# Kernel tuning notes

Hardware: AMD Instinct MI355X
Metric: run time of the kernel (lower is better)

Reference implementation:

```python
import jax, jax.numpy as jnp
import numpy as np

# Static graph/model dims
G, NPG, N = 64, 200, 12800          # graphs, nodes/graph, total nodes
EPG, E = 1000, 64000                # edges/graph, total edges
D, H, C = 1024, 3, 1024             # feature_size, heads, out channels/head
K1, K2, K3 = 160, 80, 16            # topk sizes: ceil(.8*200), .5*160, .2*80
NEG = -1e9


def _gat(x, src, dst, mask, W, att_s, att_d, b):
    """PyG GATConv (concat heads, add_self_loops=True, leaky_relu 0.2)."""
    n = x.shape[0]
    xw = (x @ W).reshape(n, H, C)                 # [n,H,C]
    a_s = (xw * att_s).sum(-1)                    # [n,H]
    a_d = (xw * att_d).sum(-1)
    loop = jnp.arange(n, dtype=src.dtype)
    s = jnp.concatenate([src, loop])
    d = jnp.concatenate([dst, loop])
    m = jnp.concatenate([mask, jnp.ones((n,), bool)])
    logit = jax.nn.leaky_relu(a_s[s] + a_d[d], 0.2)   # [E+n,H]
    logit = jnp.where(m[:, None], logit, NEG)
    mx = jax.ops.segment_max(logit, d, num_segments=n)
    ex = jnp.where(m[:, None], jnp.exp(logit - mx[d]), 0.0)
    den = jax.ops.segment_sum(ex, d, num_segments=n)
    alpha = ex / (den[d] + 1e-16)                 # segment softmax over dst
    out = jax.ops.segment_sum(alpha[:, :, None] * xw[s], d, num_segments=n)
    return out.reshape(n, H * C) + b


def _topk(x, src, dst, mask, p, n_in, k):
    """PyG TopKPooling: score=tanh(x.p/||p||), keep top-k per graph,
    scale kept rows by score; edge filtering realized as a mask."""
    score = jnp.tanh((x @ p) / jnp.linalg.norm(p))
    vals, idx = jax.lax.top_k(score.reshape(G, n_in), k)     # [G,k]
    perm = (idx + jnp.arange(G)[:, None] * n_in).reshape(-1)
    new_x = x[perm] * vals.reshape(-1, 1)
    newid = jnp.full((G * n_in,), -1, jnp.int32).at[perm].set(
        jnp.arange(G * k, dtype=jnp.int32))
    ns, nd = newid[src], newid[dst]
    nm = mask & (ns >= 0) & (nd >= 0)
    return new_x, jnp.where(nm, ns, 0), jnp.where(nm, nd, 0), nm


def _readout(x, k):
    xg = x.reshape(G, k, C)                       # contiguous equal graphs
    return jnp.concatenate([xg.max(1), xg.mean(1)], axis=1)  # [G,2C]


def setup_inputs() -> dict:
    key = jax.random.key(0)
    ks = jax.random.split(key, 32)
    x = jax.random.normal(ks[0], (N, D), jnp.float32)
    gid = jnp.repeat(jnp.arange(G, dtype=jnp.int32), EPG)
    src = jax.random.randint(ks[1], (E,), 0, NPG, jnp.int32) + gid * NPG
    dst = jax.random.randint(ks[2], (E,), 0, NPG, jnp.int32) + gid * NPG
    edge_index = jnp.stack([src, dst])
    batch_index = jnp.repeat(jnp.arange(G, dtype=jnp.int32), NPG)
    edge_attr = jnp.zeros((E, 1), jnp.float32)

    def gl(k, shape, fan):
        return jax.random.normal(k, shape, jnp.float32) * (1.0 / np.sqrt(fan))

    inp = dict(x=x, edge_attr=edge_attr, edge_index=edge_index,
               batch_index=batch_index)
    i = 3
    for L, fin in ((1, D), (2, C), (3, C)):
        inp[f'W{L}'] = gl(ks[i], (fin, H * C), fin); i += 1
        inp[f'as{L}'] = gl(ks[i], (H, C), C); i += 1
        inp[f'ad{L}'] = gl(ks[i], (H, C), C); i += 1
        inp[f'b{L}'] = jnp.zeros((H * C,), jnp.float32)
        inp[f'Wt{L}'] = gl(ks[i], (H * C, C), H * C); i += 1
        inp[f'bt{L}'] = jnp.zeros((C,), jnp.float32)
        inp[f'p{L}'] = gl(ks[i], (C,), C); i += 1
    inp['Wl1'] = gl(ks[i], (2 * C, 1024), 2 * C); i += 1
    inp['bl1'] = jnp.zeros((1024,), jnp.float32)
    inp['Wl2'] = gl(ks[i], (1024, 2), 1024); i += 1
    inp['bl2'] = jnp.zeros((2,), jnp.float32)
    return inp


def reference(x, edge_attr, edge_index, batch_index,
              W1, as1, ad1, b1, Wt1, bt1, p1,
              W2, as2, ad2, b2, Wt2, bt2, p2,
              W3, as3, ad3, b3, Wt3, bt3, p3,
              Wl1, bl1, Wl2, bl2):
    src, dst = edge_index[0], edge_index[1]
    mask = jnp.ones((src.shape[0],), bool)
    h = _gat(x, src, dst, mask, W1, as1, ad1, b1) @ Wt1 + bt1
    h, src, dst, mask = _topk(h, src, dst, mask, p1, NPG, K1)
    r1 = _readout(h, K1)
    h = _gat(h, src, dst, mask, W2, as2, ad2, b2) @ Wt2 + bt2
    h, src, dst, mask = _topk(h, src, dst, mask, p2, K1, K2)
    r2 = _readout(h, K2)
    h = _gat(h, src, dst, mask, W3, as3, ad3, b3) @ Wt3 + bt3
    h, src, dst, mask = _topk(h, src, dst, mask, p3, K2, K3)
    r3 = _readout(h, K3)
    z = r1 + r2 + r3                               # [G, 2C]
    z = jax.nn.relu(z @ Wl1 + bl1)                 # dropout inactive (eval)
    return z @ Wl2 + bl2                           # [G, 2]
```

## Files before the change

### kernel.cpp

```cpp
#include <hip/hip_runtime.h>
#include <math.h>

#define NG 64
#define EE 64000
#define HC3 3072
#define CC 1024

static inline int cdiv(int a, int b) { return (a + b - 1) / b; }

typedef float f4_t __attribute__((ext_vector_type(4)));
typedef short s8_t __attribute__((ext_vector_type(8)));

__device__ __forceinline__ float lrelu(float x) { return x > 0.f ? x : 0.2f * x; }
__device__ __forceinline__ unsigned fenc(float f) {
    unsigned u = __float_as_uint(f);
    return (u & 0x80000000u) ? ~u : (u | 0x80000000u);
}
__device__ __forceinline__ float fdec(unsigned e) {
    return (e & 0x80000000u) ? __uint_as_float(e ^ 0x80000000u) : __uint_as_float(~e);
}
__device__ __forceinline__ unsigned short f2bf(float f) {
    unsigned u = __float_as_uint(f);
    u += 0x7fffu + ((u >> 16) & 1u);
    return (unsigned short)(u >> 16);
}
__device__ __forceinline__ float bf2f(unsigned short h) {
    return __uint_as_float(((unsigned)h) << 16);
}
__device__ __forceinline__ void gll16(const unsigned short* g, unsigned short* l) {
    __builtin_amdgcn_global_load_lds(
        (const __attribute__((address_space(1))) void*)g,
        (__attribute__((address_space(3))) void*)l, 16, 0, 0);
}

__global__ __launch_bounds__(256) void gemm_prep(
    const unsigned short* __restrict__ Ahi, const unsigned short* __restrict__ Alo,
    const unsigned short* __restrict__ Bhi, const unsigned short* __restrict__ Blo,
    unsigned short* __restrict__ ohi, unsigned short* __restrict__ olo, int K)
{
    __shared__ unsigned short sAH[128 * 32];
    __shared__ unsigned short sAL[128 * 32];
    __shared__ unsigned short sBH[128 * 32];
    __shared__ unsigned short sBL[128 * 32];

    const size_t MSZ = (size_t)CC * CC;
    const int slot = blockIdx.z;
    const int lrel = slot / 3, hh = slot % 3;
    Ahi += slot * MSZ; Alo += slot * MSZ;
    Bhi += slot * MSZ; Blo += slot * MSZ;

    const int t = threadIdx.x;
    const int w = t >> 6, lane = t & 63;
    const int wr = w >> 1, wc = w & 1;
    const int row0 = blockIdx.y * 128, col0 = blockIdx.x * 128;

    const int srow = w * 16 + (lane >> 2);
    const int skg = (((lane & 3) ^ ((lane >> 3) & 3)) << 3);
    const size_t aoff0 = (size_t)(row0 + srow) * CC + skg;
    const size_t aoff1 = (size_t)(row0 + 64 + srow) * CC + skg;
    const size_t boff0 = (size_t)(col0 + srow) * CC + skg;
    const size_t boff1 = (size_t)(col0 + 64 + srow) * CC + skg;
    const int l0 = (w * 16) * 32;
    const int l1 = (64 + w * 16) * 32;

    f4_t acc[4][4];
    const f4_t z4 = {0.f, 0.f, 0.f, 0.f};
#pragma unroll
    for (int i = 0; i < 4; ++i)
#pragma unroll
        for (int j = 0; j < 4; ++j) acc[i][j] = z4;

    const int mrow0 = wr * 64 + (lane & 15);
    const int nrow0 = wc * 64 + (lane & 15);
    const int kslot = (((lane >> 4) ^ ((lane >> 1) & 3)) << 3);

    for (int k0 = 0; k0 < K; k0 += 32) {
        gll16(Ahi + aoff0 + k0, &sAH[l0]);
        gll16(Ahi + aoff1 + k0, &sAH[l1]);
        gll16(Alo + aoff0 + k0, &sAL[l0]);
        gll16(Alo + aoff1 + k0, &sAL[l1]);
        gll16(Bhi + boff0 + k0, &sBH[l0]);
        gll16(Bhi + boff1 + k0, &sBH[l1]);
        gll16(Blo + boff0 + k0, &sBL[l0]);
        gll16(Blo + boff1 + k0, &sBL[l1]);
        __syncthreads();

        s8_t ah[4], al[4], bh[4], bl[4];
#pragma unroll
        for (int mt = 0; mt < 4; ++mt) {
            ah[mt] = *(const s8_t*)&sAH[(mrow0 + mt * 16) * 32 + kslot];
            al[mt] = *(const s8_t*)&sAL[(mrow0 + mt * 16) * 32 + kslot];
        }
#pragma unroll
        for (int nt = 0; nt < 4; ++nt) {
            bh[nt] = *(const s8_t*)&sBH[(nrow0 + nt * 16) * 32 + kslot];
            bl[nt] = *(const s8_t*)&sBL[(nrow0 + nt * 16) * 32 + kslot];
        }
#pragma unroll
        for (int mt = 0; mt < 4; ++mt)
#pragma unroll
            for (int nt = 0; nt < 4; ++nt) {
                acc[mt][nt] = __builtin_amdgcn_mfma_f32_16x16x32_bf16(ah[mt], bh[nt], acc[mt][nt], 0, 0, 0);
                acc[mt][nt] = __builtin_amdgcn_mfma_f32_16x16x32_bf16(ah[mt], bl[nt], acc[mt][nt], 0, 0, 0);
                acc[mt][nt] = __builtin_amdgcn_mfma_f32_16x16x32_bf16(al[mt], bh[nt], acc[mt][nt], 0, 0, 0);
            }
        __syncthreads();
    }

#pragma unroll
    for (int mt = 0; mt < 4; ++mt) {
        int row = row0 + wr * 64 + mt * 16 + (lane >> 4) * 4;
#pragma unroll
        for (int nt = 0; nt < 4; ++nt) {
            int col = col0 + wc * 64 + nt * 16 + (lane & 15);
#pragma unroll
            for (int r = 0; r < 4; ++r) {
                float v = acc[mt][nt][r];
                unsigned short hv = f2bf(v);
                size_t dst = (size_t)lrel * 3 * MSZ + (size_t)(row + r) * HC3 + hh * CC + col;
                ohi[dst] = hv;
                olo[dst] = f2bf(v - bf2f(hv));
            }
        }
    }
}

__global__ __launch_bounds__(256) void gemm_splitk(
    const unsigned short* __restrict__ Ahi, const unsigned short* __restrict__ Alo, int lda,
    const unsigned short* __restrict__ Bhi, const unsigned short* __restrict__ Blo, int ldb,
    float* __restrict__ C, int ldc, int ksub)
{
    __shared__ unsigned short sAH[128 * 32];
    __shared__ unsigned short sAL[128 * 32];
    __shared__ unsigned short sBH[128 * 32];
    __shared__ unsigned short sBL[128 * 32];

    const int t = threadIdx.x;
    const int w = t >> 6, lane = t & 63;
    const int wr = w >> 1, wc = w & 1;
    const int row0 = blockIdx.x * 128, col0 = blockIdx.y * 128;
    const int kbase = blockIdx.z * ksub;

    const int srow = w * 16 + (lane >> 2);
    const int skg = (((lane & 3) ^ ((lane >> 3) & 3)) << 3);
    const size_t aoff0 = (size_t)(row0 + srow) * lda + skg;
    const size_t aoff1 = (size_t)(row0 + 64 + srow) * lda + skg;
    const size_t boff0 = (size_t)(col0 + srow) * ldb + skg;
    const size_t boff1 = (size_t)(col0 + 64 + srow) * ldb + skg;
    const int l0 = (w * 16) * 32;
    const int l1 = (64 + w * 16) * 32;

    f4_t acc[4][4];
    const f4_t z4 = {0.f, 0.f, 0.f, 0.f};
#pragma unroll
    for (int i = 0; i < 4; ++i)
#pragma unroll
        for (int j = 0; j < 4; ++j) acc[i][j] = z4;

    const int mrow0 = wr * 64 + (lane & 15);
    const int nrow0 = wc * 64 + (lane & 15);
    const int kslot = (((lane >> 4) ^ ((lane >> 1) & 3)) << 3);

    for (int k0 = kbase; k0 < kbase + ksub; k0 += 32) {
        gll16(Ahi + aoff0 + k0, &sAH[l0]);
        gll16(Ahi + aoff1 + k0, &sAH[l1]);
        gll16(Alo + aoff0 + k0, &sAL[l0]);
        gll16(Alo + aoff1 + k0, &sAL[l1]);
        gll16(Bhi + boff0 + k0, &sBH[l0]);
        gll16(Bhi + boff1 + k0, &sBH[l1]);
        gll16(Blo + boff0 + k0, &sBL[l0]);
        gll16(Blo + boff1 + k0, &sBL[l1]);
        __syncthreads();

        s8_t ah[4], al[4], bh[4], bl[4];
#pragma unroll
        for (int mt = 0; mt < 4; ++mt) {
            ah[mt] = *(const s8_t*)&sAH[(mrow0 + mt * 16) * 32 + kslot];
            al[mt] = *(const s8_t*)&sAL[(mrow0 + mt * 16) * 32 + kslot];
        }
#pragma unroll
        for (int nt = 0; nt < 4; ++nt) {
            bh[nt] = *(const s8_t*)&sBH[(nrow0 + nt * 16) * 32 + kslot];
            bl[nt] = *(const s8_t*)&sBL[(nrow0 + nt * 16) * 32 + kslot];
        }
#pragma unroll
        for (int mt = 0; mt < 4; ++mt)
#pragma unroll
            for (int nt = 0; nt < 4; ++nt) {
                acc[mt][nt] = __builtin_amdgcn_mfma_f32_16x16x32_bf16(ah[mt], bh[nt], acc[mt][nt], 0, 0, 0);
                acc[mt][nt] = __builtin_amdgcn_mfma_f32_16x16x32_bf16(ah[mt], bl[nt], acc[mt][nt], 0, 0, 0);
                acc[mt][nt] = __builtin_amdgcn_mfma_f32_16x16x32_bf16(al[mt], bh[nt], acc[mt][nt], 0, 0, 0);
            }
        __syncthreads();
    }

#pragma unroll
    for (int mt = 0; mt < 4; ++mt) {
        int row = row0 + wr * 64 + mt * 16 + (lane >> 4) * 4;
#pragma unroll
        for (int nt = 0; nt < 4; ++nt) {
            int col = col0 + wc * 64 + nt * 16 + (lane & 15);
#pragma unroll
            for (int r = 0; r < 4; ++r)
                atomicAdd(&C[(size_t)(row + r) * ldc + col], acc[mt][nt][r]);
        }
    }
}

__global__ void split_w_all(const float* __restrict__ w0, const float* __restrict__ w1,
    const float* __restrict__ w2, int lbase,
    unsigned short* __restrict__ ohi, unsigned short* __restrict__ olo)
{
    const float* Wp[3] = {w0, w1, w2};
    int slot = blockIdx.y;
    int L = lbase + slot / 3, h = slot % 3;
    int idx = blockIdx.x * 256 + threadIdx.x;
    int r = idx >> 10, c = idx & 1023;
    float v = Wp[L][(size_t)r * HC3 + h * CC + c];
    unsigned short hh = f2bf(v);
    ohi[(size_t)slot * 1048576 + idx] = hh;
    olo[(size_t)slot * 1048576 + idx] = f2bf(v - bf2f(hh));
}

__global__ void transpose_split_wt_all(const float* __restrict__ w0,
    const float* __restrict__ w1, const float* __restrict__ w2, int lbase,
    unsigned short* __restrict__ ohi, unsigned short* __restrict__ olo)
{
    const float* Wp[3] = {w0, w1, w2};
    int slot = blockIdx.z;
    int L = lbase + slot / 3, h = slot % 3;
    __shared__ float tile[32][33];
    int t = threadIdx.x, tr = t >> 5, tc = t & 31;
    int r0 = blockIdx.y * 32, c0 = blockIdx.x * 32;
    const float* in = Wp[L] + (size_t)h * 1048576;
#pragma unroll
    for (int i = 0; i < 4; ++i)
        tile[tr + i * 8][tc] = in[(size_t)(r0 + tr + i * 8) * CC + c0 + tc];
    __syncthreads();
    unsigned short* oh = ohi + (size_t)slot * 1048576;
    unsigned short* ol = olo + (size_t)slot * 1048576;
#pragma unroll
    for (int i = 0; i < 4; ++i) {
        int oc = c0 + tr + i * 8;
        int orr = r0 + tc;
        float v = tile[tc][tr + i * 8];
        unsigned short hh = f2bf(v);
        oh[(size_t)oc * CC + orr] = hh;
        ol[(size_t)oc * CC + orr] = f2bf(v - bf2f(hh));
    }
}

__global__ __launch_bounds__(256) void wtp_all(const float* __restrict__ wt0,
    const float* __restrict__ wt1, const float* __restrict__ wt2,
    const float* __restrict__ p0, const float* __restrict__ p1, const float* __restrict__ p2,
    int lbase, float* __restrict__ U)
{
    const float* Wp[3] = {wt0, wt1, wt2};
    const float* Pp[3] = {p0, p1, p2};
    int wid = blockIdx.x * 4 + (threadIdx.x >> 6);
    int lane = threadIdx.x & 63;
    int L = lbase + wid / HC3, rr = wid % HC3;
    const float* row = Wp[L] + (size_t)rr * CC;
    const float* p = Pp[L];
    float s = 0.f;
    for (int c = lane; c < CC; c += 64) s += row[c] * p[c];
    for (int off = 32; off; off >>= 1) s += __shfl_xor(s, off, 64);
    if (lane == 0) U[(size_t)L * HC3 + rr] = s;
}

__global__ __launch_bounds__(256) void attvec_all(const float* __restrict__ w0,
    const float* __restrict__ w1, const float* __restrict__ w2,
    const float* __restrict__ as0, const float* __restrict__ as1, const float* __restrict__ as2,
    const float* __restrict__ ad0, const float* __restrict__ ad1, const float* __restrict__ ad2,
    const float* __restrict__ U, int lbase,
    float* __restrict__ asv, float* __restrict__ adv, float* __restrict__ qv)
{
    const float* Wp[3] = {w0, w1, w2};
    const float* Sp[3] = {as0, as1, as2};
    const float* Dp[3] = {ad0, ad1, ad2};
    int L = lbase + blockIdx.y;
    int wid = blockIdx.x * 4 + (threadIdx.x >> 6);
    int lane = threadIdx.x & 63;
    int h = wid >> 10, kk = wid & 1023;
    const float* wr = Wp[L] + (long long)kk * HC3 + h * CC;
    const float* sa = Sp[L] + h * CC;
    const float* da = Dp[L] + h * CC;
    const float* ua = U + (size_t)L * HC3 + h * CC;
    float ss = 0.f, dd = 0.f, qq = 0.f;
    for (int c = lane; c < CC; c += 64) {
        float w = wr[c];
        ss += w * sa[c]; dd += w * da[c]; qq += w * ua[c];
    }
    for (int off = 32; off; off >>= 1) {
        ss += __shfl_xor(ss, off, 64); dd += __shfl_xor(dd, off, 64); qq += __shfl_xor(qq, off, 64);
    }
    if (lane == 0) {
        asv[(size_t)L * HC3 + h * CC + kk] = ss;
        adv[(size_t)L * HC3 + h * CC + kk] = dd;
        qv[(size_t)L * HC3 + h * CC + kk] = qq;
    }
}

__global__ __launch_bounds__(256) void attn_node(const float* __restrict__ xin,
    const float* __restrict__ asv, const float* __restrict__ adv, const float* __restrict__ q,
    float* __restrict__ AS, float* __restrict__ AD, float* __restrict__ T3,
    float* __restrict__ sl, unsigned* __restrict__ mxe, float* __restrict__ sexp,
    int* __restrict__ cnt, int* __restrict__ cur, int n)
{
    int node = blockIdx.x * 4 + (threadIdx.x >> 6);
    int lane = threadIdx.x & 63;
    if (node >= n) return;
    const float* xr = xin + (long long)node * CC;
    float s0 = 0, s1 = 0, s2 = 0, d0 = 0, d1 = 0, d2 = 0, t0 = 0, t1 = 0, t2 = 0;
    for (int j = lane; j < CC; j += 64) {
        float v = xr[j];
        s0 += v * asv[j]; s1 += v * asv[CC + j]; s2 += v * asv[2 * CC + j];
        d0 += v * adv[j]; d1 += v * adv[CC + j]; d2 += v * adv[2 * CC + j];
        t0 += v * q[j];   t1 += v * q[CC + j];   t2 += v * q[2 * CC + j];
    }
    for (int off = 32; off; off >>= 1) {
        s0 += __shfl_xor(s0, off, 64); s1 += __shfl_xor(s1, off, 64); s2 += __shfl_xor(s2, off, 64);
        d0 += __shfl_xor(d0, off, 64); d1 += __shfl_xor(d1, off, 64); d2 += __shfl_xor(d2, off, 64);
        t0 += __shfl_xor(t0, off, 64); t1 += __shfl_xor(t1, off, 64); t2 += __shfl_xor(t2, off, 64);
    }
    if (lane == 0) {
        AS[node * 3 + 0] = s0; AS[node * 3 + 1] = s1; AS[node * 3 + 2] = s2;
        AD[node * 3 + 0] = d0; AD[node * 3 + 1] = d1; AD[node * 3 + 2] = d2;
        T3[node * 3 + 0] = t0; T3[node * 3 + 1] = t1; T3[node * 3 + 2] = t2;
        float l0v = lrelu(s0 + d0), l1v = lrelu(s1 + d1), l2v = lrelu(s2 + d2);
        sl[node * 3 + 0] = l0v; sl[node * 3 + 1] = l1v; sl[node * 3 + 2] = l2v;
        mxe[node * 3 + 0] = fenc(l0v); mxe[node * 3 + 1] = fenc(l1v); mxe[node * 3 + 2] = fenc(l2v);
        sexp[node * 3 + 0] = 0.f; sexp[node * 3 + 1] = 0.f; sexp[node * 3 + 2] = 0.f;
        cnt[node] = 0; cur[node] = 0;
    }
}

__global__ void bvinit_pnorm(const float* __restrict__ bt0, const float* __restrict__ bt1,
    const float* __restrict__ bt2, const float* __restrict__ p0, const float* __restrict__ p1,
    const float* __restrict__ p2, int lbase, float* __restrict__ BV, float* __restrict__ PN)
{
    const float* Bp[3] = {bt0, bt1, bt2};
    const float* Pp[3] = {p0, p1, p2};
    int L = lbase + blockIdx.y;
    if (blockIdx.x < 4) {
        int c = blockIdx.x * 256 + threadIdx.x;
        BV[(size_t)L * CC + c] = Bp[L][c];
    } else {
        __shared__ float red[256];
        int t = threadIdx.x;
        const float* p = Pp[L];
        float s = 0.f;
        for (int j = t; j < CC; j += 256) { float v = p[j]; s += v * v; }
        red[t] = s; __syncthreads();
        for (int off = 128; off; off >>= 1) { if (t < off) red[t] += red[t + off]; __syncthreads(); }
        if (t == 0) PN[L] = sqrtf(red[0]);
    }
}

__global__ void bvec_part(const float* __restrict__ b0, const float* __restrict__ b1,
    const float* __restrict__ b2, const float* __restrict__ wt0, const float* __restrict__ wt1,
    const float* __restrict__ wt2, int lbase, float* __restrict__ BV)
{
    const float* bp[3] = {b0, b1, b2};
    const float* wp[3] = {wt0, wt1, wt2};
    int L = lbase + blockIdx.z;
    int c = blockIdx.x * 256 + threadIdx.x;
    int k0 = blockIdx.y * 256;
    const float* b = bp[L];
    const float* Wt = wp[L];
    float acc = 0.f;
#pragma unroll 8
    for (int k = k0; k < k0 + 256; ++k) acc += b[k] * Wt[(size_t)k * CC + c];
    atomicAdd(&BV[(size_t)L * CC + c], acc);
}

__global__ void bvp_all(const float* __restrict__ BV, const float* __restrict__ p0,
    const float* __restrict__ p1, const float* __restrict__ p2, int lbase,
    float* __restrict__ BVP)
{
    const float* Pp[3] = {p0, p1, p2};
    int L = lbase + blockIdx.x;
    __shared__ float red[256];
    int t = threadIdx.x;
    const float* p = Pp[L];
    float s = 0.f;
    for (int j = t; j < CC; j += 256) s += BV[(size_t)L * CC + j] * p[j];
    red[t] = s; __syncthreads();
    for (int off = 128; off; off >>= 1) { if (t < off) red[t] += red[t + off]; __syncthreads(); }
    if (t == 0) BVP[L] = red[0];
}

__global__ void edge_pass1(const int* __restrict__ src, const int* __restrict__ dst,
    const int* __restrict__ msk, const float* __restrict__ AS, const float* __restrict__ AD,
    unsigned* __restrict__ mxe, float* __restrict__ sexp, int* __restrict__ cnt)
{
    int e = blockIdx.x * 256 + threadIdx.x;
    if (e >= EE || !msk[e]) return;
    int s = src[e], d = dst[e];
    atomicAdd(&cnt[d], 1);
#pragma unroll
    for (int h = 0; h < 3; ++h) {
        float l = lrelu(AS[s * 3 + h] + AD[d * 3 + h]);
        atomicMax(&mxe[d * 3 + h], fenc(l));
        atomicAdd(&sexp[d * 3 + h], expf(l));
    }
}

__global__ __launch_bounds__(64) void scan_graph(const int* __restrict__ cnt,
    int* __restrict__ offs, int* __restrict__ gt, int npg)
{
    int g = blockIdx.x, lane = threadIdx.x;
    int run = 0;
    for (int c0 = 0; c0 < npg; c0 += 64) {
        int i = c0 + lane;
        int v = (i < npg) ? cnt[g * npg + i] : 0;
        int s = v;
#pragma unroll
        for (int off = 1; off < 64; off <<= 1) {
            int o = __shfl_up(s, off, 64);
            if (lane >= off) s += o;
        }
        if (i < npg) offs[g * npg + i] = run + s - v;
        run += __shfl(s, 63, 64);
    }
    if (lane == 0) gt[g] = run;
}

__global__ void post_edge(int* __restrict__ offs, const int* __restrict__ gt,
    const unsigned* __restrict__ mxe, const float* __restrict__ sl,
    const float* __restrict__ sexp, float* __restrict__ mxf, float* __restrict__ den,
    int n, int npg)
{
    int i = blockIdx.x * 256 + threadIdx.x;
    if (i >= n) return;
    int g = i / npg;
    int base = 0;
    for (int gg = 0; gg < g; ++gg) base += gt[gg];
    offs[i] += base;
#pragma unroll
    for (int h = 0; h < 3; ++h) {
        float m = fdec(mxe[i * 3 + h]);
        mxf[i * 3 + h] = m;
        den[i * 3 + h] = expf(sl[i * 3 + h] - m) + expf(-m) * sexp[i * 3 + h];
    }
}

__global__ void fill_alpha(const int* __restrict__ src, const int* __restrict__ dst,
    const int* __restrict__ msk, const int* __restrict__ offs, int* __restrict__ cur,
    const float* __restrict__ AS, const float* __restrict__ AD,
    const float* __restrict__ mxf, const float* __restrict__ den,
    int* __restrict__ csrs, float* __restrict__ csra)
{
    int e = blockIdx.x * 256 + threadIdx.x;
    if (e >= EE || !msk[e]) return;
    int s = src[e], d = dst[e];
    int pos = offs[d] + atomicAdd(&cur[d], 1);
    csrs[pos] = s;
#pragma unroll
    for (int h = 0; h < 3; ++h) {
        float l = lrelu(AS[s * 3 + h] + AD[d * 3 + h]);
        float ex = expf(l - mxf[d * 3 + h]);
        csra[pos * 3 + h] = ex / (den[d * 3 + h] + 1e-16f);
    }
}

__global__ __launch_bounds__(64) void score_topk(const float* __restrict__ T3,
    const float* __restrict__ sl, const float* __restrict__ mxf, const float* __restrict__ den,
    const int* __restrict__ offs, const int* __restrict__ cnt, const int* __restrict__ csrs,
    const float* __restrict__ csra, const float* __restrict__ bvp, const float* __restrict__ pn,
    int npg, int k, int* __restrict__ perm, float* __restrict__ vals, int* __restrict__ newid)
{
    __shared__ float sc[256];
    int g = blockIdx.x, lane = threadIdx.x;
    float bv0 = bvp[0], pn0 = pn[0];
    for (int ii = lane; ii < npg; ii += 64) {
        int i = g * npg + ii;
        float s = 0.f;
#pragma unroll
        for (int h = 0; h < 3; ++h) {
            float aself = expf(sl[i * 3 + h] - mxf[i * 3 + h]) / (den[i * 3 + h] + 1e-16f);
            s += aself * T3[i * 3 + h];
        }
        int beg = offs[i], num = cnt[i];
        for (int e = 0; e < num; ++e) {
            int sn = csrs[beg + e];
#pragma unroll
            for (int h = 0; h < 3; ++h) s += csra[(beg + e) * 3 + h] * T3[sn * 3 + h];
        }
        sc[ii] = tanhf((s + bv0) / pn0);
        newid[i] = -1;
    }
    __syncthreads();
    float v[4];
    int nsl = (npg + 63) >> 6;
#pragma unroll
    for (int s2 = 0; s2 < 4; ++s2) {
        int idx = lane + (s2 << 6);
        v[s2] = (s2 < nsl && idx < npg) ? sc[idx] : -1e30f;
    }
    for (int j = 0; j < k; ++j) {
        float bv = -2e30f; int bi = 0x7fffffff;
#pragma unroll
        for (int s2 = 0; s2 < 4; ++s2) {
            int idx = lane + (s2 << 6);
            if (v[s2] > bv) { bv = v[s2]; bi = idx; }
        }
        for (int off = 32; off; off >>= 1) {
            float ov = __shfl_xor(bv, off, 64);
            int   oi = __shfl_xor(bi, off, 64);
            if (ov > bv || (ov == bv && oi < bi)) { bv = ov; bi = oi; }
        }
        if (lane == 0) {
            perm[g * k + j] = g * npg + bi;
            vals[g * k + j] = bv;
            newid[g * npg + bi] = g * k + j;
        }
        if ((bi & 63) == lane) v[bi >> 6] = -1e30f;
    }
}

__global__ __launch_bounds__(256) void aggregate_sel(const float* __restrict__ xin,
    const float* __restrict__ sl, const float* __restrict__ mxf, const float* __restrict__ den,
    const int* __restrict__ offs, const int* __restrict__ cnt,
    const int* __restrict__ csrs, const float* __restrict__ csra,
    const int* __restrict__ perm,
    unsigned short* __restrict__ ahi, unsigned short* __restrict__ alo)
{
    int r = blockIdx.x, t = threadIdx.x;
    int i = perm[r];
    float aself[3];
#pragma unroll
    for (int h = 0; h < 3; ++h)
        aself[h] = expf(sl[i * 3 + h] - mxf[i * 3 + h]) / (den[i * 3 + h] + 1e-16f);
    const float* xr = xin + (long long)i * CC;
    float acc[3][4];
#pragma unroll
    for (int j = 0; j < 4; ++j) {
        float v = xr[t + (j << 8)];
#pragma unroll
        for (int h = 0; h < 3; ++h) acc[h][j] = aself[h] * v;
    }
    int beg = offs[i], num = cnt[i];
    for (int e = 0; e < num; ++e) {
        int s = csrs[beg + e];
        float a0 = csra[(beg + e) * 3 + 0];
        float a1 = csra[(beg + e) * 3 + 1];
        float a2 = csra[(beg + e) * 3 + 2];
        const float* sr = xin + (long long)s * CC;
#pragma unroll
        for (int j = 0; j < 4; ++j) {
            float v = sr[t + (j << 8)];
            acc[0][j] += a0 * v; acc[1][j] += a1 * v; acc[2][j] += a2 * v;
        }
    }
#pragma unroll
    for (int h = 0; h < 3; ++h)
#pragma unroll
        for (int j = 0; j < 4; ++j) {
            int c = t + (j << 8);
            float v = acc[h][j];
            unsigned short hh = f2bf(v);
            size_t idx = (size_t)r * HC3 + h * CC + c;
            ahi[idx] = hh;
            alo[idx] = f2bf(v - bf2f(hh));
        }
}

__global__ void remap_edges(int* __restrict__ s, int* __restrict__ d,
    int* __restrict__ m, const int* __restrict__ newid)
{
    int e = blockIdx.x * 256 + threadIdx.x;
    if (e >= EE) return;
    if (!m[e]) { s[e] = 0; d[e] = 0; return; }
    int ns = newid[s[e]], nd = newid[d[e]];
    int nm = (ns >= 0 && nd >= 0) ? 1 : 0;
    m[e] = nm; s[e] = nm ? ns : 0; d[e] = nm ? nd : 0;
}

__global__ __launch_bounds__(256) void readout_part(float* __restrict__ xn,
    const float* __restrict__ BV, const float* __restrict__ vals,
    int k, float* __restrict__ PM, float* __restrict__ PS)
{
    int g = blockIdx.x, ch = blockIdx.y, t = threadIdx.x;
    int rpc = k >> 3, r0 = ch * rpc;
#pragma unroll
    for (int j = 0; j < 4; ++j) {
        int c = t + (j << 8);
        float bvc = BV[c];
        float mx = -1e30f, sm = 0.f;
        for (int r = r0; r < r0 + rpc; ++r) {
            size_t idx = ((size_t)(g * k + r)) * CC + c;
            float vv = (xn[idx] + bvc) * vals[g * k + r];
            xn[idx] = vv;
            mx = fmaxf(mx, vv); sm += vv;
        }
        PM[(size_t)(g * 8 + ch) * CC + c] = mx;
        PS[(size_t)(g * 8 + ch) * CC + c] = sm;
    }
}

__global__ __launch_bounds__(256) void readout_fin(const float* __restrict__ PM,
    const float* __restrict__ PS, int k, float* __restrict__ R)
{
    int g = blockIdx.x, t = threadIdx.x;
#pragma unroll
    for (int j = 0; j < 4; ++j) {
        int c = t + (j << 8);
        float mx = -1e30f, sm = 0.f;
#pragma unroll
        for (int ch = 0; ch < 8; ++ch) {
            mx = fmaxf(mx, PM[(size_t)(g * 8 + ch) * CC + c]);
            sm += PS[(size_t)(g * 8 + ch) * CC + c];
        }
        R[g * 2048 + c] = mx;
        R[g * 2048 + 1024 + c] = sm / (float)k;
    }
}

__global__ void copy_edges(const int* __restrict__ ei, int* __restrict__ s,
    int* __restrict__ d, int* __restrict__ m)
{
    int e = blockIdx.x * 256 + threadIdx.x;
    if (e >= EE) return;
    s[e] = ei[e]; d[e] = ei[EE + e]; m[e] = 1;
}

__global__ __launch_bounds__(256) void mlp1_kernel(const float* __restrict__ R0,
    const float* __restrict__ R1, const float* __restrict__ R2,
    const float* __restrict__ Wl1, const float* __restrict__ bl1, float* __restrict__ Z1)
{
    int c = blockIdx.x * 256 + threadIdx.x;
    int g = blockIdx.y;
    float acc = bl1[c];
    const float* r0 = R0 + g * 2048;
    const float* r1 = R1 + g * 2048;
    const float* r2 = R2 + g * 2048;
    for (int kk = 0; kk < 2048; ++kk)
        acc += (r0[kk] + r1[kk] + r2[kk]) * Wl1[kk * 1024 + c];
    Z1[g * 1024 + c] = acc > 0.f ? acc : 0.f;
}

__global__ __launch_bounds__(64) void mlp2_kernel(const float* __restrict__ Z1,
    const float* __restrict__ Wl2, const float* __restrict__ bl2, float* __restrict__ out)
{
    int b = blockIdx.x; int g = b >> 1, o = b & 1;
    int lane = threadIdx.x;
    const float* zr = Z1 + g * 1024;
    float s = 0.f;
    for (int j = lane; j < 1024; j += 64) s += zr[j] * Wl2[j * 2 + o];
    for (int off = 32; off; off >>= 1) s += __shfl_xor(s, off, 64);
    if (lane == 0) out[g * 2 + o] = s + bl2[o];
}

extern "C" void kernel_launch(void* const* d_in, const int* in_sizes, int n_in,
                              void* d_out, int out_size, void* d_ws, size_t ws_size,
                              hipStream_t stream)
{
    const float* x   = (const float*)d_in[0];
    const int*   ei  = (const int*)d_in[2];
    const float* W[3]    = {(const float*)d_in[4],  (const float*)d_in[11], (const float*)d_in[18]};
    const float* atts[3] = {(const float*)d_in[5],  (const float*)d_in[12], (const float*)d_in[19]};
    const float* attd[3] = {(const float*)d_in[6],  (const float*)d_in[13], (const float*)d_in[20]};
    const float* bb[3]   = {(const float*)d_in[7],  (const float*)d_in[14], (const float*)d_in[21]};
    const float* Wt[3]   = {(const float*)d_in[8],  (const float*)d_in[15], (const float*)d_in[22]};
    const float* bt[3]   = {(const float*)d_in[9],  (const float*)d_in[16], (const float*)d_in[23]};
    const float* pv[3]   = {(const float*)d_in[10], (const float*)d_in[17], (const float*)d_in[24]};
    const float* Wl1 = (const float*)d_in[25];
    const float* bl1 = (const float*)d_in[26];
    const float* Wl2 = (const float*)d_in[27];
    const float* bl2 = (const float*)d_in[28];
    float* out = (float*)d_out;

    const bool batched = ws_size >= (size_t)225 * 1024 * 1024;

    char* wp = (char*)d_ws;
    auto carve = [&](size_t bytes) -> void* {
        void* p = (void*)wp;
        wp += (bytes + 255) & ~(size_t)255;
        return p;
    };
    const int NMAX = 12800;
    const int GKMAX = 10240;
    const size_t MSZ = (size_t)CC * CC;
    const int NSLOT = batched ? 9 : 3;
    unsigned short* A2H = (unsigned short*)carve((size_t)GKMAX * HC3 * 2);
    unsigned short* A2L = (unsigned short*)carve((size_t)GKMAX * HC3 * 2);
    unsigned short* WTH = (unsigned short*)A2H;
    unsigned short* WTL = WTH + (size_t)NSLOT * MSZ;
    unsigned short* WSH = WTL + (size_t)NSLOT * MSZ;
    unsigned short* WSL = (unsigned short*)A2L;
    float* XN   = (float*)carve((size_t)GKMAX * CC * 4);
    unsigned short* B2H = (unsigned short*)carve((size_t)NSLOT * MSZ * 2);
    unsigned short* B2L = (unsigned short*)carve((size_t)NSLOT * MSZ * 2);
    float* PM   = (float*)carve((size_t)NG * 8 * CC * 4);
    float* PS   = (float*)carve((size_t)NG * 8 * CC * 4);
    float* ASV  = (float*)carve((size_t)3 * HC3 * 4);
    float* ADV  = (float*)carve((size_t)3 * HC3 * 4);
    float* QV   = (float*)carve((size_t)3 * HC3 * 4);
    float* UU   = (float*)carve((size_t)3 * HC3 * 4);
    float* BV   = (float*)carve((size_t)3 * CC * 4);
    float* AS   = (float*)carve((size_t)NMAX * 3 * 4);
    float* AD   = (float*)carve((size_t)NMAX * 3 * 4);
    float* T3   = (float*)carve((size_t)NMAX * 3 * 4);
    float* SL   = (float*)carve((size_t)NMAX * 3 * 4);
    unsigned* MXE = (unsigned*)carve((size_t)NMAX * 3 * 4);
    float* MXF  = (float*)carve((size_t)NMAX * 3 * 4);
    float* DEN  = (float*)carve((size_t)NMAX * 3 * 4);
    float* SEXP = (float*)carve((size_t)NMAX * 3 * 4);
    int* CNT    = (int*)carve((size_t)NMAX * 4);
    int* OFFS   = (int*)carve((size_t)NMAX * 4);
    int* CUR    = (int*)carve((size_t)NMAX * 4);
    int* NEWID  = (int*)carve((size_t)NMAX * 4);
    int* GT     = (int*)carve((size_t)NG * 4);
    int* CSRS   = (int*)carve((size_t)EE * 4);
    float* CSRA = (float*)carve((size_t)EE * 3 * 4);
    int* SRC = (int*)carve((size_t)EE * 4);
    int* DST = (int*)carve((size_t)EE * 4);
    int* MK  = (int*)carve((size_t)EE * 4);
    int* PERM  = (int*)carve((size_t)GKMAX * 4);
    float* VALS = (float*)carve((size_t)GKMAX * 4);
    float* PN  = (float*)carve(256);
    float* BVP = (float*)carve(256);
    float* R0 = (float*)carve((size_t)NG * 2048 * 4);
    float* R1 = (float*)carve((size_t)NG * 2048 * 4);
    float* R2 = (float*)carve((size_t)NG * 2048 * 4);
    float* Z1 = (float*)carve((size_t)NG * 1024 * 4);
    float* Rarr[3] = {R0, R1, R2};
    (void)in_sizes; (void)n_in; (void)out_size;

    copy_edges<<<cdiv(EE, 256), 256, 0, stream>>>(ei, SRC, DST, MK);

    auto prep = [&](int lbase, int nl) {
        int nslots = 3 * nl;
        split_w_all<<<dim3(4096, nslots), 256, 0, stream>>>(W[0], W[1], W[2], lbase, WSH, WSL);
        transpose_split_wt_all<<<dim3(32, 32, nslots), 256, 0, stream>>>(Wt[0], Wt[1], Wt[2],
                                                                          lbase, WTH, WTL);
        wtp_all<<<nl * 768, 256, 0, stream>>>(Wt[0], Wt[1], Wt[2], pv[0], pv[1], pv[2],
                                              lbase, UU);
        gemm_prep<<<dim3(8, 8, nslots), 256, 0, stream>>>(WTH, WTL, WSH, WSL, B2H, B2L, CC);
        attvec_all<<<dim3(768, nl), 256, 0, stream>>>(W[0], W[1], W[2],
            atts[0], atts[1], atts[2], attd[0], attd[1], attd[2], UU, lbase, ASV, ADV, QV);
        bvinit_pnorm<<<dim3(5, nl), 256, 0, stream>>>(bt[0], bt[1], bt[2],
            pv[0], pv[1], pv[2], lbase, BV, PN);
        bvec_part<<<dim3(4, 12, nl), 256, 0, stream>>>(bb[0], bb[1], bb[2],
            Wt[0], Wt[1], Wt[2], lbase, BV);
        bvp_all<<<nl, 256, 0, stream>>>(BV, pv[0], pv[1], pv[2], lbase, BVP);
    };

    if (batched) prep(0, 3);

    const int ns_[3]  = {12800, 10240, 5120};
    const int npg_[3] = {200, 160, 80};
    const int kk_[3]  = {160, 80, 16};
    const int sk_[3]  = {2, 2, 4};
    const float* xin = x;

    for (int L = 0; L < 3; ++L) {
        int n = ns_[L], npg = npg_[L], k = kk_[L];
        int gk = NG * k;
        if (!batched) prep(L, 1);
        size_t b2off = batched ? (size_t)L * 3 * MSZ : 0;
        attn_node<<<n / 4, 256, 0, stream>>>(xin, ASV + (size_t)L * HC3,
            ADV + (size_t)L * HC3, QV + (size_t)L * HC3, AS, AD, T3,
            SL, MXE, SEXP, CNT, CUR, n);
        edge_pass1<<<cdiv(EE, 256), 256, 0, stream>>>(SRC, DST, MK, AS, AD, MXE, SEXP, CNT);
        scan_graph<<<NG, 64, 0, stream>>>(CNT, OFFS, GT, npg);
        post_edge<<<cdiv(n, 256), 256, 0, stream>>>(OFFS, GT, MXE, SL, SEXP, MXF, DEN, n, npg);
        fill_alpha<<<cdiv(EE, 256), 256, 0, stream>>>(SRC, DST, MK, OFFS, CUR,
                                                      AS, AD, MXF, DEN, CSRS, CSRA);
        score_topk<<<NG, 64, 0, stream>>>(T3, SL, MXF, DEN, OFFS, CNT, CSRS, CSRA,
                                          BVP + L, PN + L, npg, k, PERM, VALS, NEWID);
        aggregate_sel<<<gk, 256, 0, stream>>>(xin, SL, MXF, DEN, OFFS, CNT, CSRS, CSRA,
                                              PERM, A2H, A2L);
        hipMemsetAsync(XN, 0, (size_t)gk * CC * 4, stream);
        gemm_splitk<<<dim3(gk / 128, 8, sk_[L]), 256, 0, stream>>>(A2H, A2L, HC3,
            B2H + b2off, B2L + b2off, HC3, XN, CC, HC3 / sk_[L]);
        readout_part<<<dim3(NG, 8), 256, 0, stream>>>(XN, BV + (size_t)L * CC, VALS,
                                                      k, PM, PS);
        readout_fin<<<NG, 256, 0, stream>>>(PM, PS, k, Rarr[L]);
        if (L < 2) remap_edges<<<cdiv(EE, 256), 256, 0, stream>>>(SRC, DST, MK, NEWID);
        xin = XN;
    }

    mlp1_kernel<<<dim3(4, NG), 256, 0, stream>>>(R0, R1, R2, Wl1, bl1, Z1);
    mlp2_kernel<<<NG * 2, 64, 0, stream>>>(Z1, Wl2, bl2, out);
}
```

Measured before the change: 1.335 ms.

## Replace CSR build with fixed-degree adjacency slots and recompute attention on the fly

Drops the scan/post-edge/fill-alpha kernels: edges are written directly into per-node fixed MAXDEG slots during the first edge pass, and attention coefficients are recomputed from AS/AD/max/sum in score_topk and aggregate_sel. Edge remapping for the next layer is folded into edge_pass1. This removes several small kernel launches and the CSR alpha buffer. It risks silently dropping edges if any node's in-degree exceeds 64, though the running sums still count every edge.

```diff
diff --git a/kernel.cpp b/kernel.cpp
--- a/kernel.cpp
+++ b/kernel.cpp
@@ -5,6 +5,7 @@
 #define EE 64000
 #define HC3 3072
 #define CC 1024
+#define MAXDEG 64
 
 static inline int cdiv(int a, int b) { return (a + b - 1) / b; }
 
@@ -305,7 +306,7 @@
     const float* __restrict__ asv, const float* __restrict__ adv, const float* __restrict__ q,
     float* __restrict__ AS, float* __restrict__ AD, float* __restrict__ T3,
     float* __restrict__ sl, unsigned* __restrict__ mxe, float* __restrict__ sexp,
-    int* __restrict__ cnt, int* __restrict__ cur, int n)
+    int* __restrict__ cnt, int n)
 {
     int node = blockIdx.x * 4 + (threadIdx.x >> 6);
     int lane = threadIdx.x & 63;
@@ -331,7 +332,7 @@
         sl[node * 3 + 0] = l0v; sl[node * 3 + 1] = l1v; sl[node * 3 + 2] = l2v;
         mxe[node * 3 + 0] = fenc(l0v); mxe[node * 3 + 1] = fenc(l1v); mxe[node * 3 + 2] = fenc(l2v);
         sexp[node * 3 + 0] = 0.f; sexp[node * 3 + 1] = 0.f; sexp[node * 3 + 2] = 0.f;
-        cnt[node] = 0; cur[node] = 0;
+        cnt[node] = 0;
     }
 }
 
@@ -390,14 +391,29 @@
     if (t == 0) BVP[L] = red[0];
 }
 
-__global__ void edge_pass1(const int* __restrict__ src, const int* __restrict__ dst,
-    const int* __restrict__ msk, const float* __restrict__ AS, const float* __restrict__ AD,
-    unsigned* __restrict__ mxe, float* __restrict__ sexp, int* __restrict__ cnt)
+__global__ void edge_pass1(int* __restrict__ src, int* __restrict__ dst,
+    int* __restrict__ msk, const int* __restrict__ newid,
+    const float* __restrict__ AS, const float* __restrict__ AD,
+    unsigned* __restrict__ mxe, float* __restrict__ sexp, int* __restrict__ cnt,
+    int* __restrict__ csrs)
 {
     int e = blockIdx.x * 256 + threadIdx.x;
-    if (e >= EE || !msk[e]) return;
-    int s = src[e], d = dst[e];
-    atomicAdd(&cnt[d], 1);
+    if (e >= EE) return;
+    int m = msk[e];
+    int s, d;
+    if (newid) {
+        if (!m) { src[e] = 0; dst[e] = 0; return; }
+        int ns = newid[src[e]], nd = newid[dst[e]];
+        int nm = (ns >= 0 && nd >= 0) ? 1 : 0;
+        msk[e] = nm; src[e] = nm ? ns : 0; dst[e] = nm ? nd : 0;
+        if (!nm) return;
+        s = ns; d = nd;
+    } else {
+        if (!m) return;
+        s = src[e]; d = dst[e];
+    }
+    int slot = atomicAdd(&cnt[d], 1);
+    if (slot < MAXDEG) csrs[d * MAXDEG + slot] = s;
 #pragma unroll
     for (int h = 0; h < 3; ++h) {
         float l = lrelu(AS[s * 3 + h] + AD[d * 3 + h]);
@@ -406,68 +422,11 @@
     }
 }
 
-__global__ __launch_bounds__(64) void scan_graph(const int* __restrict__ cnt,
-    int* __restrict__ offs, int* __restrict__ gt, int npg)
-{
-    int g = blockIdx.x, lane = threadIdx.x;
-    int run = 0;
-    for (int c0 = 0; c0 < npg; c0 += 64) {
-        int i = c0 + lane;
-        int v = (i < npg) ? cnt[g * npg + i] : 0;
-        int s = v;
-#pragma unroll
-        for (int off = 1; off < 64; off <<= 1) {
-            int o = __shfl_up(s, off, 64);
-            if (lane >= off) s += o;
-        }
-        if (i < npg) offs[g * npg + i] = run + s - v;
-        run += __shfl(s, 63, 64);
-    }
-    if (lane == 0) gt[g] = run;
-}
-
-__global__ void post_edge(int* __restrict__ offs, const int* __restrict__ gt,
-    const unsigned* __restrict__ mxe, const float* __restrict__ sl,
-    const float* __restrict__ sexp, float* __restrict__ mxf, float* __restrict__ den,
-    int n, int npg)
-{
-    int i = blockIdx.x * 256 + threadIdx.x;
-    if (i >= n) return;
-    int g = i / npg;
-    int base = 0;
-    for (int gg = 0; gg < g; ++gg) base += gt[gg];
-    offs[i] += base;
-#pragma unroll
-    for (int h = 0; h < 3; ++h) {
-        float m = fdec(mxe[i * 3 + h]);
-        mxf[i * 3 + h] = m;
-        den[i * 3 + h] = expf(sl[i * 3 + h] - m) + expf(-m) * sexp[i * 3 + h];
-    }
-}
-
-__global__ void fill_alpha(const int* __restrict__ src, const int* __restrict__ dst,
-    const int* __restrict__ msk, const int* __restrict__ offs, int* __restrict__ cur,
-    const float* __restrict__ AS, const float* __restrict__ AD,
-    const float* __restrict__ mxf, const float* __restrict__ den,
-    int* __restrict__ csrs, float* __restrict__ csra)
-{
-    int e = blockIdx.x * 256 + threadIdx.x;
-    if (e >= EE || !msk[e]) return;
-    int s = src[e], d = dst[e];
-    int pos = offs[d] + atomicAdd(&cur[d], 1);
-    csrs[pos] = s;
-#pragma unroll
-    for (int h = 0; h < 3; ++h) {
-        float l = lrelu(AS[s * 3 + h] + AD[d * 3 + h]);
-        float ex = expf(l - mxf[d * 3 + h]);
-        csra[pos * 3 + h] = ex / (den[d * 3 + h] + 1e-16f);
-    }
-}
-
 __global__ __launch_bounds__(64) void score_topk(const float* __restrict__ T3,
-    const float* __restrict__ sl, const float* __restrict__ mxf, const float* __restrict__ den,
-    const int* __restrict__ offs, const int* __restrict__ cnt, const int* __restrict__ csrs,
-    const float* __restrict__ csra, const float* __restrict__ bvp, const float* __restrict__ pn,
+    const float* __restrict__ sl, const unsigned* __restrict__ mxe,
+    const float* __restrict__ sexp, const float* __restrict__ AS,
+    const float* __restrict__ AD, const int* __restrict__ cnt, const int* __restrict__ csrs,
+    const float* __restrict__ bvp, const float* __restrict__ pn,
     int npg, int k, int* __restrict__ perm, float* __restrict__ vals, int* __restrict__ newid)
 {
     __shared__ float sc[256];
@@ -476,16 +435,25 @@
     for (int ii = lane; ii < npg; ii += 64) {
         int i = g * npg + ii;
         float s = 0.f;
+        float mxf3[3], rden3[3], ad3[3];
 #pragma unroll
         for (int h = 0; h < 3; ++h) {
-            float aself = expf(sl[i * 3 + h] - mxf[i * 3 + h]) / (den[i * 3 + h] + 1e-16f);
-            s += aself * T3[i * 3 + h];
-        }
-        int beg = offs[i], num = cnt[i];
+            float m = fdec(mxe[i * 3 + h]);
+            float es = expf(sl[i * 3 + h] - m);
+            float den = es + expf(-m) * sexp[i * 3 + h];
+            mxf3[h] = m; rden3[h] = 1.f / (den + 1e-16f);
+            ad3[h] = AD[i * 3 + h];
+            s += es * rden3[h] * T3[i * 3 + h];
+        }
+        int num = cnt[i]; if (num > MAXDEG) num = MAXDEG;
+        int beg = i * MAXDEG;
         for (int e = 0; e < num; ++e) {
             int sn = csrs[beg + e];
 #pragma unroll
-            for (int h = 0; h < 3; ++h) s += csra[(beg + e) * 3 + h] * T3[sn * 3 + h];
+            for (int h = 0; h < 3; ++h) {
+                float l = lrelu(AS[sn * 3 + h] + ad3[h]);
+                s += expf(l - mxf3[h]) * rden3[h] * T3[sn * 3 + h];
+            }
         }
         sc[ii] = tanhf((s + bv0) / pn0);
         newid[i] = -1;
@@ -520,18 +488,36 @@
 }
 
 __global__ __launch_bounds__(256) void aggregate_sel(const float* __restrict__ xin,
-    const float* __restrict__ sl, const float* __restrict__ mxf, const float* __restrict__ den,
-    const int* __restrict__ offs, const int* __restrict__ cnt,
-    const int* __restrict__ csrs, const float* __restrict__ csra,
+    const float* __restrict__ sl, const unsigned* __restrict__ mxe,
+    const float* __restrict__ sexp, const float* __restrict__ AS,
+    const float* __restrict__ AD, const int* __restrict__ cnt, const int* __restrict__ csrs,
     const int* __restrict__ perm,
     unsigned short* __restrict__ ahi, unsigned short* __restrict__ alo)
 {
+    __shared__ float salpha[MAXDEG * 3];
+    __shared__ int ssrc[MAXDEG];
     int r = blockIdx.x, t = threadIdx.x;
     int i = perm[r];
-    float aself[3];
-#pragma unroll
-    for (int h = 0; h < 3; ++h)
-        aself[h] = expf(sl[i * 3 + h] - mxf[i * 3 + h]) / (den[i * 3 + h] + 1e-16f);
+    float mxf3[3], rden3[3], aself[3];
+#pragma unroll
+    for (int h = 0; h < 3; ++h) {
+        float m = fdec(mxe[i * 3 + h]);
+        float es = expf(sl[i * 3 + h] - m);
+        float den = es + expf(-m) * sexp[i * 3 + h];
+        mxf3[h] = m; rden3[h] = 1.f / (den + 1e-16f);
+        aself[h] = es * rden3[h];
+    }
+    int num = cnt[i]; if (num > MAXDEG) num = MAXDEG;
+    if (t < num) {
+        int sn = csrs[i * MAXDEG + t];
+        ssrc[t] = sn;
+#pragma unroll
+        for (int h = 0; h < 3; ++h) {
+            float l = lrelu(AS[sn * 3 + h] + AD[i * 3 + h]);
+            salpha[t * 3 + h] = expf(l - mxf3[h]) * rden3[h];
+        }
+    }
+    __syncthreads();
     const float* xr = xin + (long long)i * CC;
     float acc[3][4];
 #pragma unroll
@@ -540,12 +526,11 @@
 #pragma unroll
         for (int h = 0; h < 3; ++h) acc[h][j] = aself[h] * v;
     }
-    int beg = offs[i], num = cnt[i];
     for (int e = 0; e < num; ++e) {
-        int s = csrs[beg + e];
-        float a0 = csra[(beg + e) * 3 + 0];
-        float a1 = csra[(beg + e) * 3 + 1];
-        float a2 = csra[(beg + e) * 3 + 2];
+        int s = ssrc[e];
+        float a0 = salpha[e * 3 + 0];
+        float a1 = salpha[e * 3 + 1];
+        float a2 = salpha[e * 3 + 2];
         const float* sr = xin + (long long)s * CC;
 #pragma unroll
         for (int j = 0; j < 4; ++j) {
@@ -564,17 +549,6 @@
             ahi[idx] = hh;
             alo[idx] = f2bf(v - bf2f(hh));
         }
-}
-
-__global__ void remap_edges(int* __restrict__ s, int* __restrict__ d,
-    int* __restrict__ m, const int* __restrict__ newid)
-{
-    int e = blockIdx.x * 256 + threadIdx.x;
-    if (e >= EE) return;
-    if (!m[e]) { s[e] = 0; d[e] = 0; return; }
-    int ns = newid[s[e]], nd = newid[d[e]];
-    int nm = (ns >= 0 && nd >= 0) ? 1 : 0;
-    m[e] = nm; s[e] = nm ? ns : 0; d[e] = nm ? nd : 0;
 }
 
 __global__ __launch_bounds__(256) void readout_part(float* __restrict__ xn,
@@ -704,16 +678,10 @@
     float* T3   = (float*)carve((size_t)NMAX * 3 * 4);
     float* SL   = (float*)carve((size_t)NMAX * 3 * 4);
     unsigned* MXE = (unsigned*)carve((size_t)NMAX * 3 * 4);
-    float* MXF  = (float*)carve((size_t)NMAX * 3 * 4);
-    float* DEN  = (float*)carve((size_t)NMAX * 3 * 4);
     float* SEXP = (float*)carve((size_t)NMAX * 3 * 4);
     int* CNT    = (int*)carve((size_t)NMAX * 4);
-    int* OFFS   = (int*)carve((size_t)NMAX * 4);
-    int* CUR    = (int*)carve((size_t)NMAX * 4);
     int* NEWID  = (int*)carve((size_t)NMAX * 4);
-    int* GT     = (int*)carve((size_t)NG * 4);
-    int* CSRS   = (int*)carve((size_t)EE * 4);
-    float* CSRA = (float*)carve((size_t)EE * 3 * 4);
+    int* CSRS   = (int*)carve((size_t)NMAX * MAXDEG * 4);
     int* SRC = (int*)carve((size_t)EE * 4);
     int* DST = (int*)carve((size_t)EE * 4);
     int* MK  = (int*)carve((size_t)EE * 4);
@@ -762,15 +730,12 @@
         size_t b2off = batched ? (size_t)L * 3 * MSZ : 0;
         attn_node<<<n / 4, 256, 0, stream>>>(xin, ASV + (size_t)L * HC3,
             ADV + (size_t)L * HC3, QV + (size_t)L * HC3, AS, AD, T3,
-            SL, MXE, SEXP, CNT, CUR, n);
-        edge_pass1<<<cdiv(EE, 256), 256, 0, stream>>>(SRC, DST, MK, AS, AD, MXE, SEXP, CNT);
-        scan_graph<<<NG, 64, 0, stream>>>(CNT, OFFS, GT, npg);
-        post_edge<<<cdiv(n, 256), 256, 0, stream>>>(OFFS, GT, MXE, SL, SEXP, MXF, DEN, n, npg);
-        fill_alpha<<<cdiv(EE, 256), 256, 0, stream>>>(SRC, DST, MK, OFFS, CUR,
-                                                      AS, AD, MXF, DEN, CSRS, CSRA);
-        score_topk<<<NG, 64, 0, stream>>>(T3, SL, MXF, DEN, OFFS, CNT, CSRS, CSRA,
+            SL, MXE, SEXP, CNT, n);
+        edge_pass1<<<cdiv(EE, 256), 256, 0, stream>>>(SRC, DST, MK,
+            (L > 0) ? NEWID : (const int*)nullptr, AS, AD, MXE, SEXP, CNT, CSRS);
+        score_topk<<<NG, 64, 0, stream>>>(T3, SL, MXE, SEXP, AS, AD, CNT, CSRS,
                                           BVP + L, PN + L, npg, k, PERM, VALS, NEWID);
-        aggregate_sel<<<gk, 256, 0, stream>>>(xin, SL, MXF, DEN, OFFS, CNT, CSRS, CSRA,
+        aggregate_sel<<<gk, 256, 0, stream>>>(xin, SL, MXE, SEXP, AS, AD, CNT, CSRS,
                                               PERM, A2H, A2L);
         hipMemsetAsync(XN, 0, (size_t)gk * CC * 4, stream);
         gemm_splitk<<<dim3(gk / 128, 8, sk_[L]), 256, 0, stream>>>(A2H, A2L, HC3,
@@ -778,7 +743,6 @@
         readout_part<<<dim3(NG, 8), 256, 0, stream>>>(XN, BV + (size_t)L * CC, VALS,
                                                       k, PM, PS);
         readout_fin<<<NG, 256, 0, stream>>>(PM, PS, k, Rarr[L]);
-        if (L < 2) remap_edges<<<cdiv(EE, 256), 256, 0, stream>>>(SRC, DST, MK, NEWID);
         xin = XN;
     }
 
```

After: 1.344 ms. About the same (+0.7%).
